# Kernel optimization log

Hardware: AMD Instinct MI355X
Metric: run time of the kernel (lower is better)

## Reference

```python
import jax, jax.numpy as jnp
import numpy as np

N_SHOTS, N_SAMPLES, IMG = 10, 192, 256
M = N_SHOTS * N_SAMPLES  # 1920 k-space samples


def _radial_traj():
    # mri-nufft initialize_2D_radial: uniform spoke angles over pi,
    # radii in [-0.5, 0.5) with N_SAMPLES points per spoke.
    r = (np.arange(N_SAMPLES) - N_SAMPLES / 2) / N_SAMPLES
    ang = np.pi * np.arange(N_SHOTS) / N_SHOTS
    kx = np.cos(ang)[:, None] * r[None, :]
    ky = np.sin(ang)[:, None] * r[None, :]
    return np.stack([kx, ky], axis=-1).reshape(-1, 2).astype(np.float32)


def _phase_mats(samples):
    # Separable NDFT phase factors: exp(-2i*pi*k_x*i), exp(-2i*pi*k_y*j)
    grid = jnp.arange(IMG, dtype=jnp.float32) - IMG / 2  # centered pixel coords
    Ax = jnp.exp(-2j * jnp.pi * samples[:, 0:1] * grid[None, :]).astype(jnp.complex64)  # (M, IMG)
    Ay = jnp.exp(-2j * jnp.pi * samples[:, 1:2] * grid[None, :]).astype(jnp.complex64)  # (M, IMG)
    return Ax, Ay


def _pipe_density(samples, n_iter=10):
    # Pipe & Menon density compensation: w <- w / |F F^H w| (density=True in gpunufft).
    Ax, Ay = _phase_mats(samples)
    w = jnp.ones(M, jnp.complex64)
    for _ in range(n_iter):
        t = Ax.conj() * w[:, None]                    # (M, IMG)
        img = jnp.einsum('mi,mj->ij', t, Ay.conj())   # F^H w, (IMG, IMG)
        back = jnp.einsum('mi,ij,mj->m', Ax, img, Ay) # F F^H w, (M,)
        w = w / jnp.maximum(jnp.abs(back), 1e-12).astype(jnp.complex64)
    return jnp.abs(w).astype(jnp.float32)


def setup_inputs() -> dict:
    key = jax.random.key(0)
    k1, k2 = jax.random.split(key)
    B, C = 64, 1
    x_real = jax.random.normal(k1, (B, C, IMG, IMG), dtype=jnp.float32)
    x_imag = jax.random.normal(k2, (B, C, IMG, IMG), dtype=jnp.float32)
    samples = jnp.asarray(_radial_traj())
    density = _pipe_density(samples)
    return {"x_real": x_real, "x_imag": x_imag, "samples": samples, "density": density}


def reference(x_real, x_imag, samples, density):
    x = (x_real + 1j * x_imag).astype(jnp.complex64)  # (B, C, IMG, IMG)
    Ax, Ay = _phase_mats(samples)
    # Forward NUFFT (type-2 NDFT): kspace[b,c,m] = sum_ij Ax[m,i] Ay[m,j] x[b,c,i,j]
    t = jnp.einsum('mi,bcij->bcmj', Ax, x)            # (B, C, M, IMG)
    kspace = jnp.einsum('mj,bcmj->bcm', Ay, t)        # (B, C, M)
    # Density-compensated adjoint NUFFT (type-1 NDFT)
    kw = kspace * density.astype(jnp.complex64)
    u = jnp.einsum('mi,bcm->bcmi', Ax.conj(), kw)     # (B, C, M, IMG)
    adj = jnp.einsum('mj,bcmi->bcij', Ay.conj(), u) / (IMG * IMG)
    return jnp.stack([adj.real, adj.imag], axis=-1)   # (B, C, IMG, IMG, 2)
```

## Files before the change

### kernel.cpp

```cpp
#include <hip/hip_runtime.h>
#include <hip/hip_bf16.h>
#include <hip/hip_fp16.h>

constexpr int IMG_ = 256;
constexpr int M_   = 1920;
constexpr int B_   = 64;
constexpr int MI_  = M_ * IMG_;
constexpr int IMG2 = IMG_ * IMG_;

typedef _Float16 half8 __attribute__((ext_vector_type(8)));
typedef float    floatx4 __attribute__((ext_vector_type(4)));

__global__ __launch_bounds__(256) void phase1_k(
    const float* __restrict__ samples,
    _Float16* __restrict__ axh_r, _Float16* __restrict__ axh_i,
    _Float16* __restrict__ ayh_r, _Float16* __restrict__ ayh_i) {
  int idx = blockIdx.x * 256 + threadIdx.x;
  if (idx >= MI_) return;
  int m = idx >> 8;
  int i = idx & 255;
  float g  = (float)i - 128.0f;
  float kx = samples[2 * m + 0];
  float ky = samples[2 * m + 1];
  float sx, cx, sy, cy;
  sincospif(-2.0f * kx * g, &sx, &cx);
  sincospif(-2.0f * ky * g, &sy, &cy);
  axh_r[idx] = (_Float16)cx; axh_i[idx] = (_Float16)sx;
  ayh_r[idx] = (_Float16)cy; ayh_i[idx] = (_Float16)sy;
}

__global__ __launch_bounds__(256) void phase2_k(
    const float* __restrict__ samples,
    _Float16* __restrict__ axtc_r, _Float16* __restrict__ axtc_i,
    _Float16* __restrict__ aytc_r, _Float16* __restrict__ aytc_i) {
  int m = blockIdx.x * 256 + threadIdx.x;
  if (m >= M_) return;
  int i = blockIdx.y;
  float g  = (float)i - 128.0f;
  float kx = samples[2 * m + 0];
  float ky = samples[2 * m + 1];
  float sx, cx, sy, cy;
  sincospif(-2.0f * kx * g, &sx, &cx);
  sincospif(-2.0f * ky * g, &sy, &cy);
  int o = i * M_ + m;
  axtc_r[o] = (_Float16)cx; axtc_i[o] = (_Float16)(-sx);
  aytc_r[o] = (_Float16)cy; aytc_i[o] = (_Float16)(-sy);
}

__global__ __launch_bounds__(256) void xt_k(
    const float* __restrict__ xr, const float* __restrict__ xi,
    _Float16* __restrict__ xth_r, _Float16* __restrict__ xth_i) {
  __shared__ float tr[32][33], ti[32][33];
  const int t = threadIdx.x;
  const int b = blockIdx.z;
  const int i0 = blockIdx.x * 32, j0 = blockIdx.y * 32;
  const int r = t >> 5, c = t & 31;
#pragma unroll
  for (int k = 0; k < 4; ++k) {
    int row = r + k * 8;
    tr[row][c] = xr[(size_t)b * IMG2 + (i0 + row) * IMG_ + j0 + c];
    ti[row][c] = xi[(size_t)b * IMG2 + (i0 + row) * IMG_ + j0 + c];
  }
  __syncthreads();
#pragma unroll
  for (int k = 0; k < 4; ++k) {
    int row = r + k * 8;
    xth_r[(size_t)b * IMG2 + (j0 + row) * IMG_ + i0 + c] = (_Float16)tr[c][row];
    xth_i[(size_t)b * IMG2 + (j0 + row) * IMG_ + i0 + c] = (_Float16)ti[c][row];
  }
}

__global__ __launch_bounds__(256) void fwd_k(
    const _Float16* __restrict__ axh_r, const _Float16* __restrict__ axh_i,
    const _Float16* __restrict__ ayh_r, const _Float16* __restrict__ ayh_i,
    const _Float16* __restrict__ xth_r, const _Float16* __restrict__ xth_i,
    const float* __restrict__ density,
    _Float16* __restrict__ kwh_r, _Float16* __restrict__ kwh_i) {
  __shared__ _Float16 asr[64 * 40], asi[64 * 40];
  __shared__ _Float16 bsr[64 * 40], bsi[64 * 40];

  const int t = threadIdx.x;
  const int w = t >> 6;
  const int l = t & 63;
  const int lr = l & 15;
  const int q  = l >> 4;
  const int b  = blockIdx.y;
  const int m0 = blockIdx.x * 64;
  const _Float16* __restrict__ xrb = xth_r + (size_t)b * IMG2;
  const _Float16* __restrict__ xib = xth_i + (size_t)b * IMG2;

  float kr[4] = {0.f, 0.f, 0.f, 0.f};
  float ki[4] = {0.f, 0.f, 0.f, 0.f};
  const floatx4 z4 = {0.f, 0.f, 0.f, 0.f};

  for (int jc = 0; jc < 4; ++jc) {
    const int j0 = jc * 64;
    floatx4 accr[4] = {z4, z4, z4, z4};
    floatx4 acci[4] = {z4, z4, z4, z4};

    for (int kt = 0; kt < 8; ++kt) {
      const int i0 = kt * 32;
      __syncthreads();
#pragma unroll
      for (int p = 0; p < 2; ++p) {
        int slot = t + p * 256;
        int row = slot >> 3, seg = slot & 7;
        *(uint2*)&asr[row * 40 + seg * 4] = *(const uint2*)&axh_r[(m0 + row) * IMG_ + i0 + seg * 4];
        *(uint2*)&asi[row * 40 + seg * 4] = *(const uint2*)&axh_i[(m0 + row) * IMG_ + i0 + seg * 4];
        *(uint2*)&bsr[row * 40 + seg * 4] = *(const uint2*)&xrb[(j0 + row) * IMG_ + i0 + seg * 4];
        *(uint2*)&bsi[row * 40 + seg * 4] = *(const uint2*)&xib[(j0 + row) * IMG_ + i0 + seg * 4];
      }
      __syncthreads();

      half8 ar = *(const half8*)&asr[(w * 16 + lr) * 40 + q * 8];
      half8 ai = *(const half8*)&asi[(w * 16 + lr) * 40 + q * 8];
      half8 nai = -ai;
#pragma unroll
      for (int jt = 0; jt < 4; ++jt) {
        half8 br = *(const half8*)&bsr[(jt * 16 + lr) * 40 + q * 8];
        half8 bi = *(const half8*)&bsi[(jt * 16 + lr) * 40 + q * 8];
        accr[jt] = __builtin_amdgcn_mfma_f32_16x16x32_f16(ar,  br, accr[jt], 0, 0, 0);
        accr[jt] = __builtin_amdgcn_mfma_f32_16x16x32_f16(nai, bi, accr[jt], 0, 0, 0);
        acci[jt] = __builtin_amdgcn_mfma_f32_16x16x32_f16(ar,  bi, acci[jt], 0, 0, 0);
        acci[jt] = __builtin_amdgcn_mfma_f32_16x16x32_f16(ai,  br, acci[jt], 0, 0, 0);
      }
    }

#pragma unroll
    for (int jt = 0; jt < 4; ++jt) {
      int j = j0 + jt * 16 + lr;
#pragma unroll
      for (int reg = 0; reg < 4; ++reg) {
        int m = m0 + w * 16 + q * 4 + reg;
        float yr = (float)ayh_r[m * IMG_ + j];
        float yi = (float)ayh_i[m * IMG_ + j];
        float tr = accr[jt][reg], ti = acci[jt][reg];
        kr[reg] = fmaf(yr, tr, fmaf(-yi, ti, kr[reg]));
        ki[reg] = fmaf(yr, ti, fmaf(yi, tr, ki[reg]));
      }
    }
  }

#pragma unroll
  for (int reg = 0; reg < 4; ++reg) {
#pragma unroll
    for (int off = 1; off < 16; off <<= 1) {
      kr[reg] += __shfl_xor(kr[reg], off);
      ki[reg] += __shfl_xor(ki[reg], off);
    }
  }
  if (lr == 0) {
#pragma unroll
    for (int reg = 0; reg < 4; ++reg) {
      int m = m0 + w * 16 + q * 4 + reg;
      float d = density[m];
      kwh_r[b * M_ + m] = (_Float16)(kr[reg] * d);
      kwh_i[b * M_ + m] = (_Float16)(ki[reg] * d);
    }
  }
}

__global__ __launch_bounds__(256) void adj_k(
    const _Float16* __restrict__ axtc_r, const _Float16* __restrict__ axtc_i,
    const _Float16* __restrict__ aytc_r, const _Float16* __restrict__ aytc_i,
    const _Float16* __restrict__ kwh_r, const _Float16* __restrict__ kwh_i,
    float* __restrict__ out) {
  __shared__ _Float16 asr[64 * 40], asi[64 * 40];
  __shared__ _Float16 wsr[64 * 40], wsi[64 * 40];

  const int t = threadIdx.x;
  const int w = t >> 6;
  const int l = t & 63;
  const int lr = l & 15;
  const int q  = l >> 4;
  const int b  = blockIdx.z;
  const int i0 = blockIdx.x * 64;
  const int j0 = blockIdx.y * 64;

  const floatx4 z4 = {0.f, 0.f, 0.f, 0.f};
  floatx4 accr[4] = {z4, z4, z4, z4};
  floatx4 acci[4] = {z4, z4, z4, z4};

  for (int mt = 0; mt < M_ / 32; ++mt) {
    const int m0 = mt * 32;
    __syncthreads();
#pragma unroll
    for (int p = 0; p < 2; ++p) {
      int slot = t + p * 256;
      int row = slot >> 3, seg = slot & 7;
      *(uint2*)&asr[row * 40 + seg * 4] = *(const uint2*)&axtc_r[(i0 + row) * M_ + m0 + seg * 4];
      *(uint2*)&asi[row * 40 + seg * 4] = *(const uint2*)&axtc_i[(i0 + row) * M_ + m0 + seg * 4];
    }
    {
      int row = t >> 2, seg = t & 3;
      const __half2* ay_r = (const __half2*)&aytc_r[(j0 + row) * M_ + m0 + seg * 8];
      const __half2* ay_i = (const __half2*)&aytc_i[(j0 + row) * M_ + m0 + seg * 8];
      const __half2* kw_r = (const __half2*)&kwh_r[b * M_ + m0 + seg * 8];
      const __half2* kw_i = (const __half2*)&kwh_i[b * M_ + m0 + seg * 8];
      __half2 wr[4], wi[4];
#pragma unroll
      for (int e = 0; e < 4; ++e) {
        __half2 yr = ay_r[e], yi = ay_i[e], cr = kw_r[e], ci = kw_i[e];
        wr[e] = __hsub2(__hmul2(cr, yr), __hmul2(ci, yi));
        wi[e] = __hfma2(cr, yi, __hmul2(ci, yr));
      }
      *(uint4*)&wsr[row * 40 + seg * 8] = *(uint4*)wr;
      *(uint4*)&wsi[row * 40 + seg * 8] = *(uint4*)wi;
    }
    __syncthreads();

    half8 ar = *(const half8*)&asr[(w * 16 + lr) * 40 + q * 8];
    half8 ai = *(const half8*)&asi[(w * 16 + lr) * 40 + q * 8];
    half8 nai = -ai;
#pragma unroll
    for (int jt = 0; jt < 4; ++jt) {
      half8 br = *(const half8*)&wsr[(jt * 16 + lr) * 40 + q * 8];
      half8 bi = *(const half8*)&wsi[(jt * 16 + lr) * 40 + q * 8];
      accr[jt] = __builtin_amdgcn_mfma_f32_16x16x32_f16(ar,  br, accr[jt], 0, 0, 0);
      accr[jt] = __builtin_amdgcn_mfma_f32_16x16x32_f16(nai, bi, accr[jt], 0, 0, 0);
      acci[jt] = __builtin_amdgcn_mfma_f32_16x16x32_f16(ar,  bi, acci[jt], 0, 0, 0);
      acci[jt] = __builtin_amdgcn_mfma_f32_16x16x32_f16(ai,  br, acci[jt], 0, 0, 0);
    }
  }

  const float s = 1.0f / (float)IMG2;
#pragma unroll
  for (int jt = 0; jt < 4; ++jt) {
    int jg = j0 + jt * 16 + lr;
#pragma unroll
    for (int reg = 0; reg < 4; ++reg) {
      int ig = i0 + w * 16 + q * 4 + reg;
      float2 v = make_float2(accr[jt][reg] * s, acci[jt][reg] * s);
      *(float2*)&out[((size_t)(b * IMG_ + ig) * IMG_ + jg) * 2] = v;
    }
  }
}

extern "C" void kernel_launch(void* const* d_in, const int* in_sizes, int n_in,
                              void* d_out, int out_size, void* d_ws, size_t ws_size,
                              hipStream_t stream) {
  (void)in_sizes; (void)n_in; (void)out_size; (void)ws_size;

  const float* xr      = (const float*)d_in[0];
  const float* xi      = (const float*)d_in[1];
  const float* samples = (const float*)d_in[2];
  const float* density = (const float*)d_in[3];
  float* out = (float*)d_out;

  _Float16* f = (_Float16*)d_ws;
  _Float16* axh_r  = f + 0 * MI_;
  _Float16* axh_i  = f + 1 * MI_;
  _Float16* ayh_r  = f + 2 * MI_;
  _Float16* ayh_i  = f + 3 * MI_;
  _Float16* axtc_r = f + 4 * MI_;
  _Float16* axtc_i = f + 5 * MI_;
  _Float16* aytc_r = f + 6 * MI_;
  _Float16* aytc_i = f + 7 * MI_;
  _Float16* kwh_r  = f + 8 * MI_;
  _Float16* kwh_i  = kwh_r + B_ * M_;

  _Float16* xth_r = (_Float16*)d_out;
  _Float16* xth_i = xth_r + (size_t)B_ * IMG2;

  phase1_k<<<(MI_ + 255) / 256, 256, 0, stream>>>(samples, axh_r, axh_i, ayh_r, ayh_i);
  phase2_k<<<dim3(8, IMG_), 256, 0, stream>>>(samples, axtc_r, axtc_i, aytc_r, aytc_i);
  xt_k<<<dim3(8, 8, B_), 256, 0, stream>>>(xr, xi, xth_r, xth_i);
  fwd_k<<<dim3(M_ / 64, B_), 256, 0, stream>>>(axh_r, axh_i, ayh_r, ayh_i,
                                               xth_r, xth_i, density, kwh_r, kwh_i);
  adj_k<<<dim3(4, 4, B_), 256, 0, stream>>>(axtc_r, axtc_i, aytc_r, aytc_i,
                                            kwh_r, kwh_i, out);
}
```

Measured before the change: 288.0 us.

## Use 128x128 tiles with 32x32 MFMA and direct global-to-LDS loads

Both the forward and adjoint GEMM kernels move from 64x64 block tiles with 16x16x32 MFMA to 128x128 tiles, where each wave computes a 64x64 subtile with 32x32x16 MFMA. Operand staging now uses global_load_lds with an XOR-swizzled LDS layout in place of padded register round-trips. The adjoint kernel now folds the kspace weights into the Ax operand instead of the Ay operand. The forward kernel reduces partial kspace sums through shared memory across the two wave columns. The aim is more operand reuse per LDS load and fewer load instructions, at the cost of fewer blocks (the adjoint grid drops to 256 blocks) and more registers per thread.

```diff
diff --git a/kernel.cpp b/kernel.cpp
--- a/kernel.cpp
+++ b/kernel.cpp
@@ -9,7 +9,13 @@
 constexpr int IMG2 = IMG_ * IMG_;
 
 typedef _Float16 half8 __attribute__((ext_vector_type(8)));
-typedef float    floatx4 __attribute__((ext_vector_type(4)));
+typedef float floatx16 __attribute__((ext_vector_type(16)));
+
+__device__ inline void gl_lds16(const void* g, void* l) {
+  __builtin_amdgcn_global_load_lds(
+      (const __attribute__((address_space(1))) unsigned int*)g,
+      (__attribute__((address_space(3))) unsigned int*)l, 16, 0, 0);
+}
 
 __global__ __launch_bounds__(256) void phase1_k(
     const float* __restrict__ samples,
@@ -70,170 +76,221 @@
   }
 }
 
-__global__ __launch_bounds__(256) void fwd_k(
+__global__ __launch_bounds__(256, 2) void fwd_k(
     const _Float16* __restrict__ axh_r, const _Float16* __restrict__ axh_i,
     const _Float16* __restrict__ ayh_r, const _Float16* __restrict__ ayh_i,
     const _Float16* __restrict__ xth_r, const _Float16* __restrict__ xth_i,
     const float* __restrict__ density,
     _Float16* __restrict__ kwh_r, _Float16* __restrict__ kwh_i) {
-  __shared__ _Float16 asr[64 * 40], asi[64 * 40];
-  __shared__ _Float16 bsr[64 * 40], bsi[64 * 40];
-
-  const int t = threadIdx.x;
-  const int w = t >> 6;
-  const int l = t & 63;
-  const int lr = l & 15;
-  const int q  = l >> 4;
+  __shared__ _Float16 sA[2 * 128 * 32];
+  __shared__ _Float16 sB[2 * 128 * 32];
+  __shared__ float kred[2][128][2];
+
+  const int t  = threadIdx.x;
+  const int w  = t >> 6, l = t & 63;
+  const int lo = l & 31, hi = l >> 5;
+  const int mw = (w & 1) * 64;
+  const int jwb = w >> 1;
+  const int jw = jwb * 64;
+  const int m0 = blockIdx.x * 128;
   const int b  = blockIdx.y;
-  const int m0 = blockIdx.x * 64;
-  const _Float16* __restrict__ xrb = xth_r + (size_t)b * IMG2;
-  const _Float16* __restrict__ xib = xth_i + (size_t)b * IMG2;
-
-  float kr[4] = {0.f, 0.f, 0.f, 0.f};
-  float ki[4] = {0.f, 0.f, 0.f, 0.f};
-  const floatx4 z4 = {0.f, 0.f, 0.f, 0.f};
-
-  for (int jc = 0; jc < 4; ++jc) {
-    const int j0 = jc * 64;
-    floatx4 accr[4] = {z4, z4, z4, z4};
-    floatx4 acci[4] = {z4, z4, z4, z4};
+
+  ((float*)kred)[t] = 0.f;
+  ((float*)kred)[t + 256] = 0.f;
+
+  const _Float16* __restrict__ xb_r = xth_r + (size_t)b * IMG2;
+  const _Float16* __restrict__ xb_i = xth_i + (size_t)b * IMG2;
+
+  const floatx16 z16 = {0.f,0.f,0.f,0.f,0.f,0.f,0.f,0.f,0.f,0.f,0.f,0.f,0.f,0.f,0.f,0.f};
+
+  for (int jc = 0; jc < 2; ++jc) {
+    const int j0 = jc * 128;
+    floatx16 accr[2][2] = {{z16, z16}, {z16, z16}};
+    floatx16 acci[2][2] = {{z16, z16}, {z16, z16}};
 
     for (int kt = 0; kt < 8; ++kt) {
       const int i0 = kt * 32;
       __syncthreads();
 #pragma unroll
       for (int p = 0; p < 2; ++p) {
-        int slot = t + p * 256;
-        int row = slot >> 3, seg = slot & 7;
-        *(uint2*)&asr[row * 40 + seg * 4] = *(const uint2*)&axh_r[(m0 + row) * IMG_ + i0 + seg * 4];
-        *(uint2*)&asi[row * 40 + seg * 4] = *(const uint2*)&axh_i[(m0 + row) * IMG_ + i0 + seg * 4];
-        *(uint2*)&bsr[row * 40 + seg * 4] = *(const uint2*)&xrb[(j0 + row) * IMG_ + i0 + seg * 4];
-        *(uint2*)&bsi[row * 40 + seg * 4] = *(const uint2*)&xib[(j0 + row) * IMG_ + i0 + seg * 4];
+        int s  = w * 2 + p;
+        int q  = s * 64 + l;
+        int r  = q >> 2;
+        int cl = (q & 3) ^ (r & 3);
+        int ga = (m0 + r) * IMG_ + i0 + cl * 8;
+        int gb = (j0 + r) * IMG_ + i0 + cl * 8;
+        gl_lds16(axh_r + ga, &sA[s * 512]);
+        gl_lds16(axh_i + ga, &sA[4096 + s * 512]);
+        gl_lds16(xb_r  + gb, &sB[s * 512]);
+        gl_lds16(xb_i  + gb, &sB[4096 + s * 512]);
       }
       __syncthreads();
 
-      half8 ar = *(const half8*)&asr[(w * 16 + lr) * 40 + q * 8];
-      half8 ai = *(const half8*)&asi[(w * 16 + lr) * 40 + q * 8];
-      half8 nai = -ai;
-#pragma unroll
-      for (int jt = 0; jt < 4; ++jt) {
-        half8 br = *(const half8*)&bsr[(jt * 16 + lr) * 40 + q * 8];
-        half8 bi = *(const half8*)&bsi[(jt * 16 + lr) * 40 + q * 8];
-        accr[jt] = __builtin_amdgcn_mfma_f32_16x16x32_f16(ar,  br, accr[jt], 0, 0, 0);
-        accr[jt] = __builtin_amdgcn_mfma_f32_16x16x32_f16(nai, bi, accr[jt], 0, 0, 0);
-        acci[jt] = __builtin_amdgcn_mfma_f32_16x16x32_f16(ar,  bi, acci[jt], 0, 0, 0);
-        acci[jt] = __builtin_amdgcn_mfma_f32_16x16x32_f16(ai,  br, acci[jt], 0, 0, 0);
-      }
-    }
-
-#pragma unroll
-    for (int jt = 0; jt < 4; ++jt) {
-      int j = j0 + jt * 16 + lr;
-#pragma unroll
-      for (int reg = 0; reg < 4; ++reg) {
-        int m = m0 + w * 16 + q * 4 + reg;
-        float yr = (float)ayh_r[m * IMG_ + j];
-        float yi = (float)ayh_i[m * IMG_ + j];
-        float tr = accr[jt][reg], ti = acci[jt][reg];
-        kr[reg] = fmaf(yr, tr, fmaf(-yi, ti, kr[reg]));
-        ki[reg] = fmaf(yr, ti, fmaf(yi, tr, ki[reg]));
-      }
-    }
-  }
-
-#pragma unroll
-  for (int reg = 0; reg < 4; ++reg) {
-#pragma unroll
-    for (int off = 1; off < 16; off <<= 1) {
-      kr[reg] += __shfl_xor(kr[reg], off);
-      ki[reg] += __shfl_xor(ki[reg], off);
-    }
-  }
-  if (lr == 0) {
-#pragma unroll
-    for (int reg = 0; reg < 4; ++reg) {
-      int m = m0 + w * 16 + q * 4 + reg;
-      float d = density[m];
-      kwh_r[b * M_ + m] = (_Float16)(kr[reg] * d);
-      kwh_i[b * M_ + m] = (_Float16)(ki[reg] * d);
-    }
-  }
-}
-
-__global__ __launch_bounds__(256) void adj_k(
+#pragma unroll
+      for (int ks = 0; ks < 2; ++ks) {
+        half8 ar[2], ai[2], nai[2], br[2], bi[2];
+#pragma unroll
+        for (int tm = 0; tm < 2; ++tm) {
+          int rt  = mw + tm * 32 + lo;
+          int off = rt * 32 + ((ks * 2 + hi) ^ (rt & 3)) * 8;
+          ar[tm]  = *(const half8*)&sA[off];
+          ai[tm]  = *(const half8*)&sA[4096 + off];
+          nai[tm] = -ai[tm];
+        }
+#pragma unroll
+        for (int tj = 0; tj < 2; ++tj) {
+          int rt  = jw + tj * 32 + lo;
+          int off = rt * 32 + ((ks * 2 + hi) ^ (rt & 3)) * 8;
+          br[tj]  = *(const half8*)&sB[off];
+          bi[tj]  = *(const half8*)&sB[4096 + off];
+        }
+#pragma unroll
+        for (int tm = 0; tm < 2; ++tm)
+#pragma unroll
+          for (int tj = 0; tj < 2; ++tj) {
+            accr[tm][tj] = __builtin_amdgcn_mfma_f32_32x32x16_f16(ar[tm],  br[tj], accr[tm][tj], 0, 0, 0);
+            accr[tm][tj] = __builtin_amdgcn_mfma_f32_32x32x16_f16(nai[tm], bi[tj], accr[tm][tj], 0, 0, 0);
+            acci[tm][tj] = __builtin_amdgcn_mfma_f32_32x32x16_f16(ar[tm],  bi[tj], acci[tm][tj], 0, 0, 0);
+            acci[tm][tj] = __builtin_amdgcn_mfma_f32_32x32x16_f16(ai[tm],  br[tj], acci[tm][tj], 0, 0, 0);
+          }
+      }
+    }
+
+#pragma unroll
+    for (int tm = 0; tm < 2; ++tm) {
+#pragma unroll
+      for (int reg = 0; reg < 16; ++reg) {
+        int row = (reg & 3) + 8 * (reg >> 2) + 4 * hi;
+        int m = m0 + mw + tm * 32 + row;
+        float wr = 0.f, wi = 0.f;
+#pragma unroll
+        for (int tj = 0; tj < 2; ++tj) {
+          int j = j0 + jw + tj * 32 + lo;
+          float yr = (float)ayh_r[m * IMG_ + j];
+          float yi = (float)ayh_i[m * IMG_ + j];
+          float tr = accr[tm][tj][reg], ti = acci[tm][tj][reg];
+          wr = fmaf(yr, tr, fmaf(-yi, ti, wr));
+          wi = fmaf(yr, ti, fmaf(yi, tr, wi));
+        }
+#pragma unroll
+        for (int off = 1; off < 32; off <<= 1) {
+          wr += __shfl_xor(wr, off);
+          wi += __shfl_xor(wi, off);
+        }
+        if (lo == 0) {
+          int ml = mw + tm * 32 + row;
+          kred[jwb][ml][0] += wr;
+          kred[jwb][ml][1] += wi;
+        }
+      }
+    }
+  }
+
+  __syncthreads();
+  if (t < 128) {
+    int m = m0 + t;
+    float rr = kred[0][t][0] + kred[1][t][0];
+    float ii = kred[0][t][1] + kred[1][t][1];
+    float d  = density[m];
+    kwh_r[b * M_ + m] = (_Float16)(rr * d);
+    kwh_i[b * M_ + m] = (_Float16)(ii * d);
+  }
+}
+
+__global__ __launch_bounds__(256, 2) void adj_k(
     const _Float16* __restrict__ axtc_r, const _Float16* __restrict__ axtc_i,
     const _Float16* __restrict__ aytc_r, const _Float16* __restrict__ aytc_i,
     const _Float16* __restrict__ kwh_r, const _Float16* __restrict__ kwh_i,
     float* __restrict__ out) {
-  __shared__ _Float16 asr[64 * 40], asi[64 * 40];
-  __shared__ _Float16 wsr[64 * 40], wsi[64 * 40];
-
-  const int t = threadIdx.x;
-  const int w = t >> 6;
-  const int l = t & 63;
-  const int lr = l & 15;
-  const int q  = l >> 4;
+  __shared__ _Float16 sA[2 * 128 * 32];
+  __shared__ _Float16 sB[2 * 128 * 32];
+
+  const int t  = threadIdx.x;
+  const int w  = t >> 6, l = t & 63;
+  const int lo = l & 31, hi = l >> 5;
+  const int iw = (w & 1) * 64;
+  const int jw = (w >> 1) * 64;
+  const int i0 = blockIdx.x * 128;
+  const int j0 = blockIdx.y * 128;
   const int b  = blockIdx.z;
-  const int i0 = blockIdx.x * 64;
-  const int j0 = blockIdx.y * 64;
-
-  const floatx4 z4 = {0.f, 0.f, 0.f, 0.f};
-  floatx4 accr[4] = {z4, z4, z4, z4};
-  floatx4 acci[4] = {z4, z4, z4, z4};
+
+  const floatx16 z16 = {0.f,0.f,0.f,0.f,0.f,0.f,0.f,0.f,0.f,0.f,0.f,0.f,0.f,0.f,0.f,0.f};
+  floatx16 accr[2][2] = {{z16, z16}, {z16, z16}};
+  floatx16 acci[2][2] = {{z16, z16}, {z16, z16}};
 
   for (int mt = 0; mt < M_ / 32; ++mt) {
     const int m0 = mt * 32;
     __syncthreads();
 #pragma unroll
     for (int p = 0; p < 2; ++p) {
-      int slot = t + p * 256;
-      int row = slot >> 3, seg = slot & 7;
-      *(uint2*)&asr[row * 40 + seg * 4] = *(const uint2*)&axtc_r[(i0 + row) * M_ + m0 + seg * 4];
-      *(uint2*)&asi[row * 40 + seg * 4] = *(const uint2*)&axtc_i[(i0 + row) * M_ + m0 + seg * 4];
-    }
-    {
-      int row = t >> 2, seg = t & 3;
-      const __half2* ay_r = (const __half2*)&aytc_r[(j0 + row) * M_ + m0 + seg * 8];
-      const __half2* ay_i = (const __half2*)&aytc_i[(j0 + row) * M_ + m0 + seg * 8];
-      const __half2* kw_r = (const __half2*)&kwh_r[b * M_ + m0 + seg * 8];
-      const __half2* kw_i = (const __half2*)&kwh_i[b * M_ + m0 + seg * 8];
-      __half2 wr[4], wi[4];
-#pragma unroll
-      for (int e = 0; e < 4; ++e) {
-        __half2 yr = ay_r[e], yi = ay_i[e], cr = kw_r[e], ci = kw_i[e];
-        wr[e] = __hsub2(__hmul2(cr, yr), __hmul2(ci, yi));
-        wi[e] = __hfma2(cr, yi, __hmul2(ci, yr));
-      }
-      *(uint4*)&wsr[row * 40 + seg * 8] = *(uint4*)wr;
-      *(uint4*)&wsi[row * 40 + seg * 8] = *(uint4*)wi;
+      int s  = w * 2 + p;
+      int q  = s * 64 + l;
+      int r  = q >> 2;
+      int cl = (q & 3) ^ (r & 3);
+      int gb = (j0 + r) * M_ + m0 + cl * 8;
+      gl_lds16(aytc_r + gb, &sB[s * 512]);
+      gl_lds16(aytc_i + gb, &sB[4096 + s * 512]);
+    }
+#pragma unroll
+    for (int p = 0; p < 2; ++p) {
+      int q  = p * 256 + t;
+      int r  = q >> 2;
+      int cl = (q & 3) ^ (r & 3);
+      int ga = (i0 + r) * M_ + m0 + cl * 8;
+      half8 xr8 = *(const half8*)&axtc_r[ga];
+      half8 xi8 = *(const half8*)&axtc_i[ga];
+      half8 kr8 = *(const half8*)&kwh_r[b * M_ + m0 + cl * 8];
+      half8 ki8 = *(const half8*)&kwh_i[b * M_ + m0 + cl * 8];
+      half8 wr8 = xr8 * kr8 - xi8 * ki8;
+      half8 wi8 = xr8 * ki8 + xi8 * kr8;
+      *(half8*)&sA[q * 8]        = wr8;
+      *(half8*)&sA[4096 + q * 8] = wi8;
     }
     __syncthreads();
 
-    half8 ar = *(const half8*)&asr[(w * 16 + lr) * 40 + q * 8];
-    half8 ai = *(const half8*)&asi[(w * 16 + lr) * 40 + q * 8];
-    half8 nai = -ai;
-#pragma unroll
-    for (int jt = 0; jt < 4; ++jt) {
-      half8 br = *(const half8*)&wsr[(jt * 16 + lr) * 40 + q * 8];
-      half8 bi = *(const half8*)&wsi[(jt * 16 + lr) * 40 + q * 8];
-      accr[jt] = __builtin_amdgcn_mfma_f32_16x16x32_f16(ar,  br, accr[jt], 0, 0, 0);
-      accr[jt] = __builtin_amdgcn_mfma_f32_16x16x32_f16(nai, bi, accr[jt], 0, 0, 0);
-      acci[jt] = __builtin_amdgcn_mfma_f32_16x16x32_f16(ar,  bi, acci[jt], 0, 0, 0);
-      acci[jt] = __builtin_amdgcn_mfma_f32_16x16x32_f16(ai,  br, acci[jt], 0, 0, 0);
+#pragma unroll
+    for (int ks = 0; ks < 2; ++ks) {
+      half8 ar[2], ai[2], nai[2], br[2], bi[2];
+#pragma unroll
+      for (int tm = 0; tm < 2; ++tm) {
+        int rt  = iw + tm * 32 + lo;
+        int off = rt * 32 + ((ks * 2 + hi) ^ (rt & 3)) * 8;
+        ar[tm]  = *(const half8*)&sA[off];
+        ai[tm]  = *(const half8*)&sA[4096 + off];
+        nai[tm] = -ai[tm];
+      }
+#pragma unroll
+      for (int tj = 0; tj < 2; ++tj) {
+        int rt  = jw + tj * 32 + lo;
+        int off = rt * 32 + ((ks * 2 + hi) ^ (rt & 3)) * 8;
+        br[tj]  = *(const half8*)&sB[off];
+        bi[tj]  = *(const half8*)&sB[4096 + off];
+      }
+#pragma unroll
+      for (int tm = 0; tm < 2; ++tm)
+#pragma unroll
+        for (int tj = 0; tj < 2; ++tj) {
+          accr[tm][tj] = __builtin_amdgcn_mfma_f32_32x32x16_f16(ar[tm],  br[tj], accr[tm][tj], 0, 0, 0);
+          accr[tm][tj] = __builtin_amdgcn_mfma_f32_32x32x16_f16(nai[tm], bi[tj], accr[tm][tj], 0, 0, 0);
+          acci[tm][tj] = __builtin_amdgcn_mfma_f32_32x32x16_f16(ar[tm],  bi[tj], acci[tm][tj], 0, 0, 0);
+          acci[tm][tj] = __builtin_amdgcn_mfma_f32_32x32x16_f16(ai[tm],  br[tj], acci[tm][tj], 0, 0, 0);
+        }
     }
   }
 
   const float s = 1.0f / (float)IMG2;
 #pragma unroll
-  for (int jt = 0; jt < 4; ++jt) {
-    int jg = j0 + jt * 16 + lr;
-#pragma unroll
-    for (int reg = 0; reg < 4; ++reg) {
-      int ig = i0 + w * 16 + q * 4 + reg;
-      float2 v = make_float2(accr[jt][reg] * s, acci[jt][reg] * s);
-      *(float2*)&out[((size_t)(b * IMG_ + ig) * IMG_ + jg) * 2] = v;
-    }
-  }
+  for (int tm = 0; tm < 2; ++tm)
+#pragma unroll
+    for (int tj = 0; tj < 2; ++tj)
+#pragma unroll
+      for (int reg = 0; reg < 16; ++reg) {
+        int row = (reg & 3) + 8 * (reg >> 2) + 4 * hi;
+        int ig = i0 + iw + tm * 32 + row;
+        int jg = j0 + jw + tj * 32 + lo;
+        float2 v = make_float2(accr[tm][tj][reg] * s, acci[tm][tj][reg] * s);
+        *(float2*)&out[((size_t)(b * IMG_ + ig) * IMG_ + jg) * 2] = v;
+      }
 }
 
 extern "C" void kernel_launch(void* const* d_in, const int* in_sizes, int n_in,
@@ -265,8 +322,8 @@
   phase1_k<<<(MI_ + 255) / 256, 256, 0, stream>>>(samples, axh_r, axh_i, ayh_r, ayh_i);
   phase2_k<<<dim3(8, IMG_), 256, 0, stream>>>(samples, axtc_r, axtc_i, aytc_r, aytc_i);
   xt_k<<<dim3(8, 8, B_), 256, 0, stream>>>(xr, xi, xth_r, xth_i);
-  fwd_k<<<dim3(M_ / 64, B_), 256, 0, stream>>>(axh_r, axh_i, ayh_r, ayh_i,
-                                               xth_r, xth_i, density, kwh_r, kwh_i);
-  adj_k<<<dim3(4, 4, B_), 256, 0, stream>>>(axtc_r, axtc_i, aytc_r, aytc_i,
+  fwd_k<<<dim3(M_ / 128, B_), 256, 0, stream>>>(axh_r, axh_i, ayh_r, ayh_i,
+                                                xth_r, xth_i, density, kwh_r, kwh_i);
+  adj_k<<<dim3(2, 2, B_), 256, 0, stream>>>(axtc_r, axtc_i, aytc_r, aytc_i,
                                             kwh_r, kwh_i, out);
 }
```

Measured after the change: 331.5 us. 1.15x slower.
